# Kernel tuning notes

Measured on AMD Instinct MI355X. Metric: run time of the kernel, lower is better.

The kernel has to match this reference:

```python
import jax, jax.numpy as jnp
import numpy as np


def setup_inputs() -> dict:
    key = jax.random.key(0)
    k1, k2, k3, k4, k5 = jax.random.split(key, 5)
    B, K, S, E, I, D = 4, 2, 512, 8, 1024, 2048
    x = jax.random.normal(k1, (B, S, I), dtype=jnp.float32)
    weights = jax.random.uniform(k2, (B, K, S), dtype=jnp.float32)
    ensembles = jax.random.randint(k3, (B, K, S), 0, E, dtype=jnp.int64)
    # xavier_uniform-style init for expert weight tables
    lim1 = float(np.sqrt(6.0 / (D + I)))
    proj_in = jax.random.uniform(k4, (E, D, I), dtype=jnp.float32, minval=-lim1, maxval=lim1)
    proj_out = jax.random.uniform(k5, (E, I, D), dtype=jnp.float32, minval=-lim1, maxval=lim1)
    return {"x": x, "weights": weights, "ensembles": ensembles,
            "proj_in": proj_in, "proj_out": proj_out}


def reference(x, weights, ensembles, proj_in, proj_out):
    # x: (B,S,I); weights/ensembles: (B,K,S); proj_in: (E,D,I); proj_out: (E,I,D)
    # Same math as the torch module (dropout = identity in eval):
    #   per token t, out = sum_k w[k,t] * W2[e_kt] @ relu(W1[e_kt] @ x[t])
    # Computed as all-expert batched GEMMs + a gated (one-hot scatter) combine,
    # which is mathematically identical and avoids the (B,K,S,D,I) gather blowup.
    E = proj_in.shape[0]
    h = jax.nn.relu(jnp.einsum('edi,bsi->bsed', proj_in, x))      # (B,S,E,D)
    o = jnp.einsum('eid,bsed->bsei', proj_out, h)                 # (B,S,E,I)
    onehot = jax.nn.one_hot(ensembles, E, dtype=x.dtype)          # (B,K,S,E)
    gate = jnp.einsum('bks,bkse->bse', weights, onehot)           # (B,S,E)
    return jnp.einsum('bsei,bse->bsi', o, gate)                   # (B,S,I)
```

## Files before the change

### kernel.cpp

```cpp
#include <hip/hip_runtime.h>
#include <stdint.h>

#define THREADS 512
#define BM 256
#define BN 128
#define BK 64
#define MAXT 24
#define NE 8
#define BB 4
#define SS 512
#define KK 2
#define II 1024
#define DD 2048
#define NTOK (BB * SS)
#define NASSIGN (BB * KK * SS)

#define CH_X (NTOK * II / 8)
#define CH_P (NE * DD * II / 8)
#define CB_X (CH_X / 256)
#define CB_P (CH_P / 256)
#define CB_TOTAL (CB_X + 2 * CB_P)

typedef unsigned short u16;
typedef __attribute__((ext_vector_type(8))) __bf16 bf16x8;
typedef __attribute__((ext_vector_type(4))) float f32x4;
typedef __attribute__((ext_vector_type(4))) unsigned int u32x4;

__device__ __forceinline__ u16 f32_to_bf16(float f) {
    unsigned int u = __builtin_bit_cast(unsigned int, f);
    unsigned int r = u + 0x7FFFu + ((u >> 16) & 1u);
    return (u16)(r >> 16);
}

__device__ __forceinline__ void gload16(const void* g, void* l) {
    __builtin_amdgcn_global_load_lds(
        (const __attribute__((address_space(1))) unsigned int*)g,
        (__attribute__((address_space(3))) unsigned int*)l, 16, 0, 0);
}

__global__ void setup_kernel(const void* __restrict__ ens_raw,
                             const float* __restrict__ weights,
                             int* __restrict__ meta,
                             int* __restrict__ tok,
                             float* __restrict__ wgt) {
    __shared__ int s_cnt[NE];
    __shared__ int s_cur[NE];
    __shared__ int s_flag;
    const int t = threadIdx.x;
    if (t < NE) s_cnt[t] = 0;
    if (t == 0) s_flag = 0;
    __syncthreads();

    const unsigned int* w32 = (const unsigned int*)ens_raw;
    unsigned int f = 0;
    for (int i = t; i < NASSIGN / 2; i += 256) f |= w32[2 * i + 1];
    if (f) atomicOr(&s_flag, 1);
    __syncthreads();
    const bool is32 = (s_flag != 0);
    const int* e32 = (const int*)ens_raw;
    const long long* e64 = (const long long*)ens_raw;

    for (int a = t; a < NASSIGN; a += 256) {
        int e = is32 ? e32[a] : (int)e64[a];
        atomicAdd(&s_cnt[e & 7], 1);
    }
    __syncthreads();

    if (t == 0) {
        int pb = 0, nt = 0;
        for (int e = 0; e < NE; e++) {
            int c = s_cnt[e];
            meta[8 + e] = c;
            meta[16 + e] = pb;
            s_cur[e] = pb;
            int n128 = (c + 127) >> 7;
            int pe = pb + n128 * 128;
            for (int i2 = 0; i2 < n128; i2 += 2) {
                meta[32 + nt] = e;
                meta[64 + nt] = pb + i2 * 128;
                meta[96 + nt] = pb + c;
                meta[128 + nt] = pe;
                nt++;
            }
            pb = pe;
        }
        meta[0] = nt;
        meta[1] = pb;
    }
    __syncthreads();

    for (int a = t; a < NASSIGN; a += 256) {
        int e = is32 ? e32[a] : (int)e64[a];
        e &= 7;
        int slot = atomicAdd(&s_cur[e], 1);
        int b = a >> 10;
        int s = a & (SS - 1);
        tok[slot] = b * SS + s;
        wgt[slot] = weights[a];
    }
    __syncthreads();

    for (int e = 0; e < NE; e++) {
        int st = meta[16 + e] + meta[8 + e];
        int en = (e < NE - 1) ? meta[16 + e + 1] : meta[1];
        for (int i = st + t; i < en; i += 256) {
            tok[i] = 0;
            wgt[i] = 0.f;
        }
    }
}

__global__ __launch_bounds__(256)
void convert3(const float* __restrict__ x,
              const float* __restrict__ pin,
              const float* __restrict__ pout,
              u16* __restrict__ xb,
              u16* __restrict__ pb1,
              u16* __restrict__ pb2) {
    const int b = blockIdx.x;
    const float* s;
    u16* d;
    int base;
    if (b < CB_X)            { s = x;    d = xb;  base = b << 8; }
    else if (b < CB_X + CB_P){ s = pin;  d = pb1; base = (b - CB_X) << 8; }
    else                     { s = pout; d = pb2; base = (b - CB_X - CB_P) << 8; }
    const size_t k = (size_t)base + threadIdx.x;
    const f32x4* s4 = (const f32x4*)s;
    f32x4 a = __builtin_nontemporal_load(&s4[2 * k]);
    f32x4 c = __builtin_nontemporal_load(&s4[2 * k + 1]);
    union { u16 u[8]; u32x4 v; } o;
    o.u[0] = f32_to_bf16(a[0]); o.u[1] = f32_to_bf16(a[1]);
    o.u[2] = f32_to_bf16(a[2]); o.u[3] = f32_to_bf16(a[3]);
    o.u[4] = f32_to_bf16(c[0]); o.u[5] = f32_to_bf16(c[1]);
    o.u[6] = f32_to_bf16(c[2]); o.u[7] = f32_to_bf16(c[3]);
    *(u32x4*)(d + 8 * k) = o.v;
}

template <int MODE>
__global__ __launch_bounds__(THREADS, 2)
void gemm256(const u16* __restrict__ Abase,
             const u16* __restrict__ Bbase,
             const int* __restrict__ meta,
             const int* __restrict__ tok,
             const float* __restrict__ wgt,
             u16* __restrict__ hdst,
             float* __restrict__ outdst) {
    constexpr int Kdim = (MODE == 0) ? II : DD;
    constexpr int NT = Kdim / BK;
    __shared__ char smem[3 * 49152];

    const int lid = blockIdx.x;
    const int g = lid & 7;
    const int i = lid >> 3;
    const int tile = g * 3 + (i % 3);
    const int colt = i / 3;
    if (tile >= meta[0]) return;

    const int e     = meta[32 + tile];
    const int sbase = meta[64 + tile];
    const int rend  = meta[96 + tile];
    const int wend  = meta[128 + tile];
    const int padmax = meta[1];
    const int colbase = colt * BN;

    const int tid = threadIdx.x;
    const int lane = tid & 63;
    const int wv = tid >> 6;
    const int wr = wv >> 1;
    const int wc = wv & 1;

    const u16* Bp = Bbase + (size_t)e * (size_t)(DD * II) + (size_t)colbase * Kdim;

    int aoff[4], boff[2], adst[4], bdst[2];
#pragma unroll
    for (int j = 0; j < 4; j++) {
        int c = j * 512 + tid;
        int row = c >> 3;
        int s = (c & 7) ^ (row & 7);
        adst[j] = c * 16;
        int slot = sbase + row;
        if (slot > padmax - 1) slot = padmax - 1;
        aoff[j] = (MODE == 0 ? tok[slot] * II : slot * DD) + s * 8;
    }
#pragma unroll
    for (int j = 0; j < 2; j++) {
        int c = j * 512 + tid;
        int row = c >> 3;
        int s = (c & 7) ^ (row & 7);
        bdst[j] = c * 16;
        boff[j] = row * Kdim + s * 8;
    }

    f32x4 acc[4][4];
#pragma unroll
    for (int m = 0; m < 4; m++)
#pragma unroll
        for (int n = 0; n < 4; n++)
            acc[m][n] = (f32x4){0.f, 0.f, 0.f, 0.f};

    auto STAGE = [&](int kt, char* buf) {
        const int kof = kt * BK;
#pragma unroll
        for (int j = 0; j < 4; j++)
            gload16(Abase + aoff[j] + kof, buf + adst[j]);
#pragma unroll
        for (int j = 0; j < 2; j++)
            gload16(Bp + boff[j] + kof, buf + 32768 + bdst[j]);
    };

    auto COMPUTE = [&](const char* buf) {
        const u16* As = (const u16*)buf;
        const u16* Bs = (const u16*)(buf + 32768);
        bf16x8 a[2][4], b[2][4];
#pragma unroll
        for (int kk = 0; kk < 2; kk++) {
#pragma unroll
            for (int m = 0; m < 4; m++) {
                int row = wr * 64 + m * 16 + (lane & 15);
                int slot = (kk * 4 + (lane >> 4)) ^ (row & 7);
                a[kk][m] = *(const bf16x8*)&As[row * 64 + slot * 8];
            }
#pragma unroll
            for (int n = 0; n < 4; n++) {
                int col = wc * 64 + n * 16 + (lane & 15);
                int slot = (kk * 4 + (lane >> 4)) ^ (col & 7);
                b[kk][n] = *(const bf16x8*)&Bs[col * 64 + slot * 8];
            }
        }
        __builtin_amdgcn_s_setprio(1);
#pragma unroll
        for (int m = 0; m < 4; m++)
#pragma unroll
            for (int n = 0; n < 4; n++) {
                acc[m][n] = __builtin_amdgcn_mfma_f32_16x16x32_bf16(
                    a[0][m], b[0][n], acc[m][n], 0, 0, 0);
                acc[m][n] = __builtin_amdgcn_mfma_f32_16x16x32_bf16(
                    a[1][m], b[1][n], acc[m][n], 0, 0, 0);
            }
        __builtin_amdgcn_s_setprio(0);
    };

    char* pA = smem;
    char* pB = smem + 49152;
    char* pC = smem + 98304;

    STAGE(0, pA);
    STAGE(1, pB);
    asm volatile("s_waitcnt vmcnt(6)" ::: "memory");
    __builtin_amdgcn_sched_barrier(0);
    __builtin_amdgcn_s_barrier();
    __builtin_amdgcn_sched_barrier(0);

#pragma unroll 1
    for (int t = 0; t < NT; ++t) {
        if (t + 2 < NT) STAGE(t + 2, pC);
        COMPUTE(pA);
        if (t + 2 < NT) {
            asm volatile("s_waitcnt vmcnt(6)" ::: "memory");
        } else if (t + 1 < NT) {
            asm volatile("s_waitcnt vmcnt(0)" ::: "memory");
        }
        __builtin_amdgcn_sched_barrier(0);
        __builtin_amdgcn_s_barrier();
        __builtin_amdgcn_sched_barrier(0);
        char* tmp = pA; pA = pB; pB = pC; pC = tmp;
    }

    if (MODE == 0) {
#pragma unroll
        for (int m = 0; m < 4; m++) {
#pragma unroll
            for (int r = 0; r < 4; r++) {
                int row = wr * 64 + m * 16 + (lane >> 4) * 4 + r;
                int slot = sbase + row;
                if (slot < wend) {
                    size_t ro = (size_t)slot * DD;
#pragma unroll
                    for (int n = 0; n < 4; n++) {
                        int col = colbase + wc * 64 + n * 16 + (lane & 15);
                        float v = acc[m][n][r];
                        v = v > 0.f ? v : 0.f;
                        hdst[ro + col] = f32_to_bf16(v);
                    }
                }
            }
        }
    } else {
#pragma unroll
        for (int m = 0; m < 4; m++) {
#pragma unroll
            for (int r = 0; r < 4; r++) {
                int row = wr * 64 + m * 16 + (lane >> 4) * 4 + r;
                int slot = sbase + row;
                if (slot < rend) {
                    float w = wgt[slot];
                    size_t obase = (size_t)tok[slot] * II;
#pragma unroll
                    for (int n = 0; n < 4; n++) {
                        int col = colbase + wc * 64 + n * 16 + (lane & 15);
                        atomicAdd(&outdst[obase + col], acc[m][n][r] * w);
                    }
                }
            }
        }
    }
}

extern "C" void kernel_launch(void* const* d_in, const int* in_sizes, int n_in,
                              void* d_out, int out_size, void* d_ws, size_t ws_size,
                              hipStream_t stream) {
    const float* x = (const float*)d_in[0];
    const float* weights = (const float*)d_in[1];
    const void* ens = d_in[2];
    const float* pin = (const float*)d_in[3];
    const float* pout = (const float*)d_in[4];
    float* out = (float*)d_out;

    char* ws = (char*)d_ws;
    int*   meta    = (int*)(ws);
    int*   tok     = (int*)(ws + 1024);
    float* wgt     = (float*)(ws + 21504);
    u16*   x_bf    = (u16*)(ws + 41984);
    u16*   pin_bf  = (u16*)(ws + 4236288);
    u16*   pout_bf = (u16*)(ws + 37790720);
    u16*   h       = (u16*)(ws + 71345152);

    setup_kernel<<<dim3(1), dim3(256), 0, stream>>>(ens, weights, meta, tok, wgt);

    hipMemsetAsync(d_out, 0, (size_t)out_size * sizeof(float), stream);

    convert3<<<dim3(CB_TOTAL), dim3(256), 0, stream>>>(x, pin, pout, x_bf, pin_bf, pout_bf);

    gemm256<0><<<dim3(8 * 3 * 16), dim3(THREADS), 0, stream>>>(
        x_bf, pin_bf, meta, tok, wgt, h, nullptr);

    gemm256<1><<<dim3(8 * 3 * 8), dim3(THREADS), 0, stream>>>(
        h, pout_bf, meta, tok, wgt, nullptr, out);
}
```

Before: 134.8 us.

## Fuse setup into convert, loop tiles per expert, narrow second GEMM tiles

```diff
diff --git a/kernel.cpp b/kernel.cpp
--- a/kernel.cpp
+++ b/kernel.cpp
@@ -3,9 +3,7 @@
 
 #define THREADS 512
 #define BM 256
-#define BN 128
 #define BK 64
-#define MAXT 24
 #define NE 8
 #define BB 4
 #define SS 512
@@ -17,9 +15,9 @@
 
 #define CH_X (NTOK * II / 8)
 #define CH_P (NE * DD * II / 8)
-#define CB_X (CH_X / 256)
-#define CB_P (CH_P / 256)
-#define CB_TOTAL (CB_X + 2 * CB_P)
+#define CVB_X (CH_X / 512)
+#define CVB_P (CH_P / 512)
+#define CVB_TOTAL (CVB_X + 2 * CVB_P)
 
 typedef unsigned short u16;
 typedef __attribute__((ext_vector_type(8))) __bf16 bf16x8;
@@ -38,11 +36,16 @@
         (__attribute__((address_space(3))) unsigned int*)l, 16, 0, 0);
 }
 
-__global__ void setup_kernel(const void* __restrict__ ens_raw,
-                             const float* __restrict__ weights,
-                             int* __restrict__ meta,
-                             int* __restrict__ tok,
-                             float* __restrict__ wgt) {
+#define BARRIER() do { \
+    __builtin_amdgcn_sched_barrier(0); \
+    __builtin_amdgcn_s_barrier(); \
+    __builtin_amdgcn_sched_barrier(0); } while (0)
+
+__device__ void setup_body(const void* __restrict__ ens_raw,
+                           const float* __restrict__ weights,
+                           int* __restrict__ meta,
+                           int* __restrict__ tok,
+                           float* __restrict__ wgt) {
     __shared__ int s_cnt[NE];
     __shared__ int s_cur[NE];
     __shared__ int s_flag;
@@ -73,15 +76,18 @@
             meta[8 + e] = c;
             meta[16 + e] = pb;
             s_cur[e] = pb;
+            meta[160 + e] = nt;
             int n128 = (c + 127) >> 7;
             int pe = pb + n128 * 128;
+            int te = 0;
             for (int i2 = 0; i2 < n128; i2 += 2) {
                 meta[32 + nt] = e;
                 meta[64 + nt] = pb + i2 * 128;
                 meta[96 + nt] = pb + c;
                 meta[128 + nt] = pe;
-                nt++;
-            }
+                nt++; te++;
+            }
+            meta[168 + e] = te;
             pb = pe;
         }
         meta[0] = nt;
@@ -111,32 +117,48 @@
 }
 
 __global__ __launch_bounds__(256)
-void convert3(const float* __restrict__ x,
-              const float* __restrict__ pin,
-              const float* __restrict__ pout,
-              u16* __restrict__ xb,
-              u16* __restrict__ pb1,
-              u16* __restrict__ pb2) {
+void convert_setup(const float* __restrict__ x,
+                   const float* __restrict__ pin,
+                   const float* __restrict__ pout,
+                   u16* __restrict__ xb,
+                   u16* __restrict__ pb1,
+                   u16* __restrict__ pb2,
+                   const void* __restrict__ ens,
+                   const float* __restrict__ weights,
+                   int* __restrict__ meta,
+                   int* __restrict__ tok,
+                   float* __restrict__ wgt) {
     const int b = blockIdx.x;
+    if (b >= CVB_TOTAL) {
+        setup_body(ens, weights, meta, tok, wgt);
+        return;
+    }
     const float* s;
     u16* d;
-    int base;
-    if (b < CB_X)            { s = x;    d = xb;  base = b << 8; }
-    else if (b < CB_X + CB_P){ s = pin;  d = pb1; base = (b - CB_X) << 8; }
-    else                     { s = pout; d = pb2; base = (b - CB_X - CB_P) << 8; }
-    const size_t k = (size_t)base + threadIdx.x;
+    size_t rel;
+    if (b < CVB_X)             { s = x;    d = xb;  rel = (size_t)b * 512; }
+    else if (b < CVB_X + CVB_P){ s = pin;  d = pb1; rel = (size_t)(b - CVB_X) * 512; }
+    else                       { s = pout; d = pb2; rel = (size_t)(b - CVB_X - CVB_P) * 512; }
+    const size_t k = rel + (size_t)threadIdx.x * 2;
     const f32x4* s4 = (const f32x4*)s;
-    f32x4 a = __builtin_nontemporal_load(&s4[2 * k]);
-    f32x4 c = __builtin_nontemporal_load(&s4[2 * k + 1]);
-    union { u16 u[8]; u32x4 v; } o;
-    o.u[0] = f32_to_bf16(a[0]); o.u[1] = f32_to_bf16(a[1]);
-    o.u[2] = f32_to_bf16(a[2]); o.u[3] = f32_to_bf16(a[3]);
-    o.u[4] = f32_to_bf16(c[0]); o.u[5] = f32_to_bf16(c[1]);
-    o.u[6] = f32_to_bf16(c[2]); o.u[7] = f32_to_bf16(c[3]);
-    *(u32x4*)(d + 8 * k) = o.v;
-}
-
-template <int MODE>
+    f32x4 a0 = __builtin_nontemporal_load(&s4[2 * k]);
+    f32x4 a1 = __builtin_nontemporal_load(&s4[2 * k + 1]);
+    f32x4 a2 = __builtin_nontemporal_load(&s4[2 * k + 2]);
+    f32x4 a3 = __builtin_nontemporal_load(&s4[2 * k + 3]);
+    union { u16 u[8]; u32x4 v; } o0, o1;
+    o0.u[0] = f32_to_bf16(a0[0]); o0.u[1] = f32_to_bf16(a0[1]);
+    o0.u[2] = f32_to_bf16(a0[2]); o0.u[3] = f32_to_bf16(a0[3]);
+    o0.u[4] = f32_to_bf16(a1[0]); o0.u[5] = f32_to_bf16(a1[1]);
+    o0.u[6] = f32_to_bf16(a1[2]); o0.u[7] = f32_to_bf16(a1[3]);
+    o1.u[0] = f32_to_bf16(a2[0]); o1.u[1] = f32_to_bf16(a2[1]);
+    o1.u[2] = f32_to_bf16(a2[2]); o1.u[3] = f32_to_bf16(a2[3]);
+    o1.u[4] = f32_to_bf16(a3[0]); o1.u[5] = f32_to_bf16(a3[1]);
+    o1.u[6] = f32_to_bf16(a3[2]); o1.u[7] = f32_to_bf16(a3[3]);
+    *(u32x4*)(d + 8 * k) = o0.v;
+    *(u32x4*)(d + 8 * k + 8) = o1.v;
+}
+
+template <int MODE, int NB>
 __global__ __launch_bounds__(THREADS, 2)
 void gemm256(const u16* __restrict__ Abase,
              const u16* __restrict__ Bbase,
@@ -147,158 +169,168 @@
              float* __restrict__ outdst) {
     constexpr int Kdim = (MODE == 0) ? II : DD;
     constexpr int NT = Kdim / BK;
-    __shared__ char smem[3 * 49152];
+    constexpr int ASZ = BM * BK * 2;
+    constexpr int BSZ = NB * BK * 2;
+    constexpr int BUFSZ = ASZ + BSZ;
+    constexpr int IB = NB / 64;
+    constexpr int NF = NB / 32;
+    __shared__ char smem[3 * BUFSZ];
 
     const int lid = blockIdx.x;
     const int g = lid & 7;
     const int i = lid >> 3;
-    const int tile = g * 3 + (i % 3);
-    const int colt = i / 3;
-    if (tile >= meta[0]) return;
-
-    const int e     = meta[32 + tile];
-    const int sbase = meta[64 + tile];
-    const int rend  = meta[96 + tile];
-    const int wend  = meta[128 + tile];
-    const int padmax = meta[1];
-    const int colbase = colt * BN;
+    const int lt = i & 3;
+    const int colt = i >> 2;
+    const int tb   = meta[160 + g];
+    const int tcnt = meta[168 + g];
+    const int colbase = colt * NB;
 
     const int tid = threadIdx.x;
     const int lane = tid & 63;
     const int wv = tid >> 6;
     const int wr = wv >> 1;
     const int wc = wv & 1;
-
-    const u16* Bp = Bbase + (size_t)e * (size_t)(DD * II) + (size_t)colbase * Kdim;
-
-    int aoff[4], boff[2], adst[4], bdst[2];
-#pragma unroll
-    for (int j = 0; j < 4; j++) {
+    const int padmax = meta[1];
+
+    const u16* Bp = Bbase + (size_t)g * (size_t)(DD * II) + (size_t)colbase * Kdim;
+
+    int boff[IB], bdst[IB];
+#pragma unroll
+    for (int j = 0; j < IB; j++) {
         int c = j * 512 + tid;
-        int row = c >> 3;
-        int s = (c & 7) ^ (row & 7);
-        adst[j] = c * 16;
-        int slot = sbase + row;
-        if (slot > padmax - 1) slot = padmax - 1;
-        aoff[j] = (MODE == 0 ? tok[slot] * II : slot * DD) + s * 8;
-    }
-#pragma unroll
-    for (int j = 0; j < 2; j++) {
-        int c = j * 512 + tid;
-        int row = c >> 3;
-        int s = (c & 7) ^ (row & 7);
+        int col = c >> 3;
+        int s = (c & 7) ^ (col & 7);
         bdst[j] = c * 16;
-        boff[j] = row * Kdim + s * 8;
-    }
-
-    f32x4 acc[4][4];
-#pragma unroll
-    for (int m = 0; m < 4; m++)
-#pragma unroll
-        for (int n = 0; n < 4; n++)
-            acc[m][n] = (f32x4){0.f, 0.f, 0.f, 0.f};
-
-    auto STAGE = [&](int kt, char* buf) {
-        const int kof = kt * BK;
-#pragma unroll
-        for (int j = 0; j < 4; j++)
-            gload16(Abase + aoff[j] + kof, buf + adst[j]);
-#pragma unroll
-        for (int j = 0; j < 2; j++)
-            gload16(Bp + boff[j] + kof, buf + 32768 + bdst[j]);
-    };
-
-    auto COMPUTE = [&](const char* buf) {
-        const u16* As = (const u16*)buf;
-        const u16* Bs = (const u16*)(buf + 32768);
-        bf16x8 a[2][4], b[2][4];
-#pragma unroll
-        for (int kk = 0; kk < 2; kk++) {
+        boff[j] = col * Kdim + s * 8;
+    }
+
+    for (int tile = tb + lt; tile < tb + tcnt; tile += 4) {
+        const int sbase = meta[64 + tile];
+        const int rend  = meta[96 + tile];
+        const int wend  = meta[128 + tile];
+
+        int aoff[4], adst[4];
+#pragma unroll
+        for (int j = 0; j < 4; j++) {
+            int c = j * 512 + tid;
+            int row = c >> 3;
+            int s = (c & 7) ^ (row & 7);
+            adst[j] = c * 16;
+            int slot = sbase + row;
+            if (slot > padmax - 1) slot = padmax - 1;
+            aoff[j] = (MODE == 0 ? tok[slot] * II : slot * DD) + s * 8;
+        }
+
+        f32x4 acc[4][NF];
+#pragma unroll
+        for (int m = 0; m < 4; m++)
+#pragma unroll
+            for (int n = 0; n < NF; n++)
+                acc[m][n] = (f32x4){0.f, 0.f, 0.f, 0.f};
+
+        auto STAGE = [&](int kt, char* buf) {
+            const int kof = kt * BK;
+#pragma unroll
+            for (int j = 0; j < 4; j++)
+                gload16(Abase + aoff[j] + kof, buf + adst[j]);
+#pragma unroll
+            for (int j = 0; j < IB; j++)
+                gload16(Bp + boff[j] + kof, buf + ASZ + bdst[j]);
+        };
+
+        auto COMPUTE = [&](const char* buf) {
+            const u16* As = (const u16*)buf;
+            const u16* Bs = (const u16*)(buf + ASZ);
+            bf16x8 a[2][4], b[2][NF];
+#pragma unroll
+            for (int kk = 0; kk < 2; kk++) {
+#pragma unroll
+                for (int m = 0; m < 4; m++) {
+                    int row = wr * 64 + m * 16 + (lane & 15);
+                    int slot = (kk * 4 + (lane >> 4)) ^ (row & 7);
+                    a[kk][m] = *(const bf16x8*)&As[row * 64 + slot * 8];
+                }
+#pragma unroll
+                for (int n = 0; n < NF; n++) {
+                    int col = wc * (NB / 2) + n * 16 + (lane & 15);
+                    int slot = (kk * 4 + (lane >> 4)) ^ (col & 7);
+                    b[kk][n] = *(const bf16x8*)&Bs[col * 64 + slot * 8];
+                }
+            }
+            asm volatile("s_waitcnt lgkmcnt(0)" ::: "memory");
+            __builtin_amdgcn_sched_barrier(0);
+            __builtin_amdgcn_s_setprio(1);
+#pragma unroll
+            for (int m = 0; m < 4; m++)
+#pragma unroll
+                for (int n = 0; n < NF; n++) {
+                    acc[m][n] = __builtin_amdgcn_mfma_f32_16x16x32_bf16(
+                        a[0][m], b[0][n], acc[m][n], 0, 0, 0);
+                    acc[m][n] = __builtin_amdgcn_mfma_f32_16x16x32_bf16(
+                        a[1][m], b[1][n], acc[m][n], 0, 0, 0);
+                }
+            __builtin_amdgcn_s_setprio(0);
+        };
+
+        char* pA = smem;
+        char* pB = smem + BUFSZ;
+        char* pC = smem + 2 * BUFSZ;
+
+        STAGE(0, pA);
+        STAGE(1, pB);
+        if constexpr (IB == 2) asm volatile("s_waitcnt vmcnt(6)" ::: "memory");
+        else                   asm volatile("s_waitcnt vmcnt(5)" ::: "memory");
+        BARRIER();
+
+#pragma unroll 1
+        for (int t = 0; t < NT; ++t) {
+            const bool st = (t + 2 < NT);
+            if (st) STAGE(t + 2, pC);
+            COMPUTE(pA);
+            if (st) {
+                if constexpr (IB == 2) asm volatile("s_waitcnt vmcnt(6)" ::: "memory");
+                else                   asm volatile("s_waitcnt vmcnt(5)" ::: "memory");
+            } else if (t + 1 < NT) {
+                asm volatile("s_waitcnt vmcnt(0)" ::: "memory");
+            }
+            BARRIER();
+            { char* tp = pA; pA = pB; pB = pC; pC = tp; }
+        }
+
+        if (MODE == 0) {
 #pragma unroll
             for (int m = 0; m < 4; m++) {
-                int row = wr * 64 + m * 16 + (lane & 15);
-                int slot = (kk * 4 + (lane >> 4)) ^ (row & 7);
-                a[kk][m] = *(const bf16x8*)&As[row * 64 + slot * 8];
-            }
-#pragma unroll
-            for (int n = 0; n < 4; n++) {
-                int col = wc * 64 + n * 16 + (lane & 15);
-                int slot = (kk * 4 + (lane >> 4)) ^ (col & 7);
-                b[kk][n] = *(const bf16x8*)&Bs[col * 64 + slot * 8];
-            }
-        }
-        __builtin_amdgcn_s_setprio(1);
-#pragma unroll
-        for (int m = 0; m < 4; m++)
-#pragma unroll
-            for (int n = 0; n < 4; n++) {
-                acc[m][n] = __builtin_amdgcn_mfma_f32_16x16x32_bf16(
-                    a[0][m], b[0][n], acc[m][n], 0, 0, 0);
-                acc[m][n] = __builtin_amdgcn_mfma_f32_16x16x32_bf16(
-                    a[1][m], b[1][n], acc[m][n], 0, 0, 0);
-            }
-        __builtin_amdgcn_s_setprio(0);
-    };
-
-    char* pA = smem;
-    char* pB = smem + 49152;
-    char* pC = smem + 98304;
-
-    STAGE(0, pA);
-    STAGE(1, pB);
-    asm volatile("s_waitcnt vmcnt(6)" ::: "memory");
-    __builtin_amdgcn_sched_barrier(0);
-    __builtin_amdgcn_s_barrier();
-    __builtin_amdgcn_sched_barrier(0);
-
-#pragma unroll 1
-    for (int t = 0; t < NT; ++t) {
-        if (t + 2 < NT) STAGE(t + 2, pC);
-        COMPUTE(pA);
-        if (t + 2 < NT) {
-            asm volatile("s_waitcnt vmcnt(6)" ::: "memory");
-        } else if (t + 1 < NT) {
-            asm volatile("s_waitcnt vmcnt(0)" ::: "memory");
-        }
-        __builtin_amdgcn_sched_barrier(0);
-        __builtin_amdgcn_s_barrier();
-        __builtin_amdgcn_sched_barrier(0);
-        char* tmp = pA; pA = pB; pB = pC; pC = tmp;
-    }
-
-    if (MODE == 0) {
-#pragma unroll
-        for (int m = 0; m < 4; m++) {
-#pragma unroll
-            for (int r = 0; r < 4; r++) {
-                int row = wr * 64 + m * 16 + (lane >> 4) * 4 + r;
-                int slot = sbase + row;
-                if (slot < wend) {
-                    size_t ro = (size_t)slot * DD;
-#pragma unroll
-                    for (int n = 0; n < 4; n++) {
-                        int col = colbase + wc * 64 + n * 16 + (lane & 15);
-                        float v = acc[m][n][r];
-                        v = v > 0.f ? v : 0.f;
-                        hdst[ro + col] = f32_to_bf16(v);
+#pragma unroll
+                for (int r = 0; r < 4; r++) {
+                    int row = wr * 64 + m * 16 + (lane >> 4) * 4 + r;
+                    int slot = sbase + row;
+                    if (slot < wend) {
+                        size_t ro = (size_t)slot * DD;
+#pragma unroll
+                        for (int n = 0; n < NF; n++) {
+                            int col = colbase + wc * (NB / 2) + n * 16 + (lane & 15);
+                            float v = acc[m][n][r];
+                            v = v > 0.f ? v : 0.f;
+                            hdst[ro + col] = f32_to_bf16(v);
+                        }
                     }
                 }
             }
-        }
-    } else {
-#pragma unroll
-        for (int m = 0; m < 4; m++) {
-#pragma unroll
-            for (int r = 0; r < 4; r++) {
-                int row = wr * 64 + m * 16 + (lane >> 4) * 4 + r;
-                int slot = sbase + row;
-                if (slot < rend) {
-                    float w = wgt[slot];
-                    size_t obase = (size_t)tok[slot] * II;
-#pragma unroll
-                    for (int n = 0; n < 4; n++) {
-                        int col = colbase + wc * 64 + n * 16 + (lane & 15);
-                        atomicAdd(&outdst[obase + col], acc[m][n][r] * w);
+        } else {
+#pragma unroll
+            for (int m = 0; m < 4; m++) {
+#pragma unroll
+                for (int r = 0; r < 4; r++) {
+                    int row = wr * 64 + m * 16 + (lane >> 4) * 4 + r;
+                    int slot = sbase + row;
+                    if (slot < rend) {
+                        float w = wgt[slot];
+                        size_t obase = (size_t)tok[slot] * II;
+#pragma unroll
+                        for (int n = 0; n < NF; n++) {
+                            int col = colbase + wc * (NB / 2) + n * 16 + (lane & 15);
+                            atomicAdd(&outdst[obase + col], acc[m][n][r] * w);
+                        }
                     }
                 }
             }
@@ -325,15 +357,14 @@
     u16*   pout_bf = (u16*)(ws + 37790720);
     u16*   h       = (u16*)(ws + 71345152);
 
-    setup_kernel<<<dim3(1), dim3(256), 0, stream>>>(ens, weights, meta, tok, wgt);
-
     hipMemsetAsync(d_out, 0, (size_t)out_size * sizeof(float), stream);
 
-    convert3<<<dim3(CB_TOTAL), dim3(256), 0, stream>>>(x, pin, pout, x_bf, pin_bf, pout_bf);
-
-    gemm256<0><<<dim3(8 * 3 * 16), dim3(THREADS), 0, stream>>>(
+    convert_setup<<<dim3(CVB_TOTAL + 1), dim3(256), 0, stream>>>(
+        x, pin, pout, x_bf, pin_bf, pout_bf, ens, weights, meta, tok, wgt);
+
+    gemm256<0, 128><<<dim3(512), dim3(THREADS), 0, stream>>>(
         x_bf, pin_bf, meta, tok, wgt, h, nullptr);
 
-    gemm256<1><<<dim3(8 * 3 * 8), dim3(THREADS), 0, stream>>>(
+    gemm256<1, 64><<<dim3(512), dim3(THREADS), 0, stream>>>(
         h, pout_bf, meta, tok, wgt, nullptr, out);
 }
```

Result: slower. 163.7 us (+21.5%).

## Enlarge first GEMM tile to 256x256, fuse setup into conversion kernel

Applied to the files above, without the earlier changes.

```diff
diff --git a/kernel.cpp b/kernel.cpp
--- a/kernel.cpp
+++ b/kernel.cpp
@@ -2,10 +2,6 @@
 #include <stdint.h>
 
 #define THREADS 512
-#define BM 256
-#define BN 128
-#define BK 64
-#define MAXT 24
 #define NE 8
 #define BB 4
 #define SS 512
@@ -15,11 +11,11 @@
 #define NTOK (BB * SS)
 #define NASSIGN (BB * KK * SS)
 
-#define CH_X (NTOK * II / 8)
-#define CH_P (NE * DD * II / 8)
-#define CB_X (CH_X / 256)
-#define CB_P (CH_P / 256)
-#define CB_TOTAL (CB_X + 2 * CB_P)
+#define F4_X (NTOK * II / 4)
+#define F4_P (NE * DD * II / 4)
+#define CVB_X (F4_X / 1024)
+#define CVB_P (F4_P / 1024)
+#define CVB_TOTAL (CVB_X + 2 * CVB_P)
 
 typedef unsigned short u16;
 typedef __attribute__((ext_vector_type(8))) __bf16 bf16x8;
@@ -32,17 +28,26 @@
     return (u16)(r >> 16);
 }
 
+__device__ __forceinline__ unsigned int pk2(float a, float b) {
+    return (unsigned int)f32_to_bf16(a) | ((unsigned int)f32_to_bf16(b) << 16);
+}
+
 __device__ __forceinline__ void gload16(const void* g, void* l) {
     __builtin_amdgcn_global_load_lds(
         (const __attribute__((address_space(1))) unsigned int*)g,
         (__attribute__((address_space(3))) unsigned int*)l, 16, 0, 0);
 }
 
-__global__ void setup_kernel(const void* __restrict__ ens_raw,
-                             const float* __restrict__ weights,
-                             int* __restrict__ meta,
-                             int* __restrict__ tok,
-                             float* __restrict__ wgt) {
+#define BARRIER() do { \
+    __builtin_amdgcn_sched_barrier(0); \
+    __builtin_amdgcn_s_barrier(); \
+    __builtin_amdgcn_sched_barrier(0); } while (0)
+
+__device__ void setup_body(const void* __restrict__ ens_raw,
+                           const float* __restrict__ weights,
+                           int* __restrict__ meta,
+                           int* __restrict__ tok,
+                           float* __restrict__ wgt) {
     __shared__ int s_cnt[NE];
     __shared__ int s_cur[NE];
     __shared__ int s_flag;
@@ -111,57 +116,198 @@
 }
 
 __global__ __launch_bounds__(256)
-void convert3(const float* __restrict__ x,
-              const float* __restrict__ pin,
-              const float* __restrict__ pout,
-              u16* __restrict__ xb,
-              u16* __restrict__ pb1,
-              u16* __restrict__ pb2) {
+void convert_setup(const float* __restrict__ x,
+                   const float* __restrict__ pin,
+                   const float* __restrict__ pout,
+                   u16* __restrict__ xb,
+                   u16* __restrict__ pb1,
+                   u16* __restrict__ pb2,
+                   const void* __restrict__ ens,
+                   const float* __restrict__ weights,
+                   int* __restrict__ meta,
+                   int* __restrict__ tok,
+                   float* __restrict__ wgt) {
     const int b = blockIdx.x;
+    if (b >= CVB_TOTAL) {
+        setup_body(ens, weights, meta, tok, wgt);
+        return;
+    }
     const float* s;
     u16* d;
-    int base;
-    if (b < CB_X)            { s = x;    d = xb;  base = b << 8; }
-    else if (b < CB_X + CB_P){ s = pin;  d = pb1; base = (b - CB_X) << 8; }
-    else                     { s = pout; d = pb2; base = (b - CB_X - CB_P) << 8; }
-    const size_t k = (size_t)base + threadIdx.x;
+    size_t base;
+    if (b < CVB_X)             { s = x;    d = xb;  base = (size_t)b * 1024; }
+    else if (b < CVB_X + CVB_P){ s = pin;  d = pb1; base = (size_t)(b - CVB_X) * 1024; }
+    else                       { s = pout; d = pb2; base = (size_t)(b - CVB_X - CVB_P) * 1024; }
     const f32x4* s4 = (const f32x4*)s;
-    f32x4 a = __builtin_nontemporal_load(&s4[2 * k]);
-    f32x4 c = __builtin_nontemporal_load(&s4[2 * k + 1]);
-    union { u16 u[8]; u32x4 v; } o;
-    o.u[0] = f32_to_bf16(a[0]); o.u[1] = f32_to_bf16(a[1]);
-    o.u[2] = f32_to_bf16(a[2]); o.u[3] = f32_to_bf16(a[3]);
-    o.u[4] = f32_to_bf16(c[0]); o.u[5] = f32_to_bf16(c[1]);
-    o.u[6] = f32_to_bf16(c[2]); o.u[7] = f32_to_bf16(c[3]);
-    *(u32x4*)(d + 8 * k) = o.v;
-}
-
-template <int MODE>
+    f32x4 v[4];
+#pragma unroll
+    for (int q = 0; q < 4; q++)
+        v[q] = __builtin_nontemporal_load(&s4[base + q * 256 + threadIdx.x]);
+#pragma unroll
+    for (int q = 0; q < 4; q++) {
+        uint2 o;
+        o.x = pk2(v[q][0], v[q][1]);
+        o.y = pk2(v[q][2], v[q][3]);
+        *(uint2*)(d + 4 * (base + q * 256 + threadIdx.x)) = o;
+    }
+}
+
 __global__ __launch_bounds__(THREADS, 2)
-void gemm256(const u16* __restrict__ Abase,
-             const u16* __restrict__ Bbase,
-             const int* __restrict__ meta,
-             const int* __restrict__ tok,
-             const float* __restrict__ wgt,
-             u16* __restrict__ hdst,
-             float* __restrict__ outdst) {
-    constexpr int Kdim = (MODE == 0) ? II : DD;
-    constexpr int NT = Kdim / BK;
-    __shared__ char smem[3 * 49152];
+void gemm1(const u16* __restrict__ Abase,
+           const u16* __restrict__ Bbase,
+           const int* __restrict__ meta,
+           const int* __restrict__ tok,
+           u16* __restrict__ hdst) {
+    constexpr int NT = II / 64;
+    constexpr int ASZ = 256 * 64 * 2;
+    constexpr int BUFSZ = 2 * ASZ;
+    __shared__ char smem[2 * BUFSZ];
 
     const int lid = blockIdx.x;
     const int g = lid & 7;
     const int i = lid >> 3;
-    const int tile = g * 3 + (i % 3);
+    const int tile = g + 8 * (i % 3);
+    const int colt = i / 3;
+    if (tile >= meta[0]) return;
+
+    const int e     = meta[32 + tile];
+    const int sbase = meta[64 + tile];
+    const int wend  = meta[128 + tile];
+    const int padmax = meta[1];
+    const int colbase = colt * 256;
+
+    const int tid = threadIdx.x;
+    const int lane = tid & 63;
+    const int wv = tid >> 6;
+    const int wr = wv >> 2;
+    const int wc = wv & 3;
+
+    const u16* Bp = Bbase + (size_t)e * (size_t)(DD * II) + (size_t)colbase * II;
+
+    int aoff[4], boff[4], cdst[4];
+#pragma unroll
+    for (int j = 0; j < 4; j++) {
+        int c = j * 512 + tid;
+        int row = c >> 3;
+        int s = (c & 7) ^ (row & 7);
+        cdst[j] = c * 16;
+        int slot = sbase + row;
+        if (slot > padmax - 1) slot = padmax - 1;
+        aoff[j] = tok[slot] * II + s * 8;
+        boff[j] = row * II + s * 8;
+    }
+
+    f32x4 acc[8][4];
+#pragma unroll
+    for (int m = 0; m < 8; m++)
+#pragma unroll
+        for (int n = 0; n < 4; n++)
+            acc[m][n] = (f32x4){0.f, 0.f, 0.f, 0.f};
+
+    auto STAGE = [&](int kt, char* buf) {
+        const int kof = kt * 64;
+#pragma unroll
+        for (int j = 0; j < 4; j++)
+            gload16(Abase + aoff[j] + kof, buf + cdst[j]);
+#pragma unroll
+        for (int j = 0; j < 4; j++)
+            gload16(Bp + boff[j] + kof, buf + ASZ + cdst[j]);
+    };
+
+    auto COMPUTE = [&](const char* buf) {
+        const u16* As = (const u16*)buf;
+        const u16* Bs = (const u16*)(buf + ASZ);
+#pragma unroll
+        for (int kk = 0; kk < 2; kk++) {
+            bf16x8 a[8], b[4];
+#pragma unroll
+            for (int m = 0; m < 8; m++) {
+                int row = wr * 128 + m * 16 + (lane & 15);
+                int slot = (kk * 4 + (lane >> 4)) ^ (row & 7);
+                a[m] = *(const bf16x8*)&As[row * 64 + slot * 8];
+            }
+#pragma unroll
+            for (int n = 0; n < 4; n++) {
+                int col = wc * 64 + n * 16 + (lane & 15);
+                int slot = (kk * 4 + (lane >> 4)) ^ (col & 7);
+                b[n] = *(const bf16x8*)&Bs[col * 64 + slot * 8];
+            }
+            asm volatile("s_waitcnt lgkmcnt(0)" ::: "memory");
+            __builtin_amdgcn_sched_barrier(0);
+            __builtin_amdgcn_s_setprio(1);
+#pragma unroll
+            for (int m = 0; m < 8; m++)
+#pragma unroll
+                for (int n = 0; n < 4; n++)
+                    acc[m][n] = __builtin_amdgcn_mfma_f32_16x16x32_bf16(
+                        a[m], b[n], acc[m][n], 0, 0, 0);
+            __builtin_amdgcn_s_setprio(0);
+        }
+    };
+
+    char* buf0 = smem;
+    char* buf1 = smem + BUFSZ;
+
+    STAGE(0, buf0);
+    asm volatile("s_waitcnt vmcnt(0)" ::: "memory");
+    BARRIER();
+
+#pragma unroll 1
+    for (int t = 0; t < NT; ++t) {
+        char* cur = (t & 1) ? buf1 : buf0;
+        char* nxt = (t & 1) ? buf0 : buf1;
+        const bool st = (t + 1 < NT);
+        if (st) STAGE(t + 1, nxt);
+        COMPUTE(cur);
+        if (st) asm volatile("s_waitcnt vmcnt(0)" ::: "memory");
+        BARRIER();
+    }
+
+#pragma unroll
+    for (int m = 0; m < 8; m++) {
+#pragma unroll
+        for (int r = 0; r < 4; r++) {
+            int row = wr * 128 + m * 16 + (lane >> 4) * 4 + r;
+            int slot = sbase + row;
+            if (slot < wend) {
+                size_t ro = (size_t)slot * DD;
+#pragma unroll
+                for (int n = 0; n < 4; n++) {
+                    int col = colbase + wc * 64 + n * 16 + (lane & 15);
+                    float v = acc[m][n][r];
+                    v = v > 0.f ? v : 0.f;
+                    hdst[ro + col] = f32_to_bf16(v);
+                }
+            }
+        }
+    }
+}
+
+__global__ __launch_bounds__(THREADS, 2)
+void gemm2(const u16* __restrict__ Abase,
+           const u16* __restrict__ Bbase,
+           const int* __restrict__ meta,
+           const int* __restrict__ tok,
+           const float* __restrict__ wgt,
+           float* __restrict__ outdst) {
+    constexpr int NT = DD / 64;
+    constexpr int ASZ = 256 * 64 * 2;
+    constexpr int BSZ = 128 * 64 * 2;
+    constexpr int BUFSZ = ASZ + BSZ;
+    __shared__ char smem[3 * BUFSZ];
+
+    const int lid = blockIdx.x;
+    const int g = lid & 7;
+    const int i = lid >> 3;
+    const int tile = g + 8 * (i % 3);
     const int colt = i / 3;
     if (tile >= meta[0]) return;
 
     const int e     = meta[32 + tile];
     const int sbase = meta[64 + tile];
     const int rend  = meta[96 + tile];
-    const int wend  = meta[128 + tile];
     const int padmax = meta[1];
-    const int colbase = colt * BN;
+    const int colbase = colt * 128;
 
     const int tid = threadIdx.x;
     const int lane = tid & 63;
@@ -169,9 +315,9 @@
     const int wr = wv >> 1;
     const int wc = wv & 1;
 
-    const u16* Bp = Bbase + (size_t)e * (size_t)(DD * II) + (size_t)colbase * Kdim;
-
-    int aoff[4], boff[2], adst[4], bdst[2];
+    const u16* Bp = Bbase + (size_t)e * (size_t)(DD * II) + (size_t)colbase * DD;
+
+    int aoff[4], adst[4], boff[2], bdst[2];
 #pragma unroll
     for (int j = 0; j < 4; j++) {
         int c = j * 512 + tid;
@@ -180,7 +326,7 @@
         adst[j] = c * 16;
         int slot = sbase + row;
         if (slot > padmax - 1) slot = padmax - 1;
-        aoff[j] = (MODE == 0 ? tok[slot] * II : slot * DD) + s * 8;
+        aoff[j] = slot * DD + s * 8;
     }
 #pragma unroll
     for (int j = 0; j < 2; j++) {
@@ -188,7 +334,7 @@
         int row = c >> 3;
         int s = (c & 7) ^ (row & 7);
         bdst[j] = c * 16;
-        boff[j] = row * Kdim + s * 8;
+        boff[j] = row * DD + s * 8;
     }
 
     f32x4 acc[4][4];
@@ -199,18 +345,18 @@
             acc[m][n] = (f32x4){0.f, 0.f, 0.f, 0.f};
 
     auto STAGE = [&](int kt, char* buf) {
-        const int kof = kt * BK;
+        const int kof = kt * 64;
 #pragma unroll
         for (int j = 0; j < 4; j++)
             gload16(Abase + aoff[j] + kof, buf + adst[j]);
 #pragma unroll
         for (int j = 0; j < 2; j++)
-            gload16(Bp + boff[j] + kof, buf + 32768 + bdst[j]);
+            gload16(Bp + boff[j] + kof, buf + ASZ + bdst[j]);
     };
 
     auto COMPUTE = [&](const char* buf) {
         const u16* As = (const u16*)buf;
-        const u16* Bs = (const u16*)(buf + 32768);
+        const u16* Bs = (const u16*)(buf + ASZ);
         bf16x8 a[2][4], b[2][4];
 #pragma unroll
         for (int kk = 0; kk < 2; kk++) {
@@ -227,6 +373,8 @@
                 b[kk][n] = *(const bf16x8*)&Bs[col * 64 + slot * 8];
             }
         }
+        asm volatile("s_waitcnt lgkmcnt(0)" ::: "memory");
+        __builtin_amdgcn_sched_barrier(0);
         __builtin_amdgcn_s_setprio(1);
 #pragma unroll
         for (int m = 0; m < 4; m++)
@@ -241,65 +389,41 @@
     };
 
     char* pA = smem;
-    char* pB = smem + 49152;
-    char* pC = smem + 98304;
+    char* pB = smem + BUFSZ;
+    char* pC = smem + 2 * BUFSZ;
 
     STAGE(0, pA);
     STAGE(1, pB);
     asm volatile("s_waitcnt vmcnt(6)" ::: "memory");
-    __builtin_amdgcn_sched_barrier(0);
-    __builtin_amdgcn_s_barrier();
-    __builtin_amdgcn_sched_barrier(0);
+    BARRIER();
 
 #pragma unroll 1
     for (int t = 0; t < NT; ++t) {
-        if (t + 2 < NT) STAGE(t + 2, pC);
+        const bool st = (t + 2 < NT);
+        if (st) STAGE(t + 2, pC);
         COMPUTE(pA);
-        if (t + 2 < NT) {
+        if (st) {
             asm volatile("s_waitcnt vmcnt(6)" ::: "memory");
         } else if (t + 1 < NT) {
             asm volatile("s_waitcnt vmcnt(0)" ::: "memory");
         }
-        __builtin_amdgcn_sched_barrier(0);
-        __builtin_amdgcn_s_barrier();
-        __builtin_amdgcn_sched_barrier(0);
-        char* tmp = pA; pA = pB; pB = pC; pC = tmp;
-    }
-
-    if (MODE == 0) {
-#pragma unroll
-        for (int m = 0; m < 4; m++) {
-#pragma unroll
-            for (int r = 0; r < 4; r++) {
-                int row = wr * 64 + m * 16 + (lane >> 4) * 4 + r;
-                int slot = sbase + row;
-                if (slot < wend) {
-                    size_t ro = (size_t)slot * DD;
-#pragma unroll
-                    for (int n = 0; n < 4; n++) {
-                        int col = colbase + wc * 64 + n * 16 + (lane & 15);
-                        float v = acc[m][n][r];
-                        v = v > 0.f ? v : 0.f;
-                        hdst[ro + col] = f32_to_bf16(v);
-                    }
-                }
-            }
-        }
-    } else {
-#pragma unroll
-        for (int m = 0; m < 4; m++) {
-#pragma unroll
-            for (int r = 0; r < 4; r++) {
-                int row = wr * 64 + m * 16 + (lane >> 4) * 4 + r;
-                int slot = sbase + row;
-                if (slot < rend) {
-                    float w = wgt[slot];
-                    size_t obase = (size_t)tok[slot] * II;
-#pragma unroll
-                    for (int n = 0; n < 4; n++) {
-                        int col = colbase + wc * 64 + n * 16 + (lane & 15);
-                        atomicAdd(&outdst[obase + col], acc[m][n][r] * w);
-                    }
+        BARRIER();
+        { char* tp = pA; pA = pB; pB = pC; pC = tp; }
+    }
+
+#pragma unroll
+    for (int m = 0; m < 4; m++) {
+#pragma unroll
+        for (int r = 0; r < 4; r++) {
+            int row = wr * 64 + m * 16 + (lane >> 4) * 4 + r;
+            int slot = sbase + row;
+            if (slot < rend) {
+                float w = wgt[slot];
+                size_t obase = (size_t)tok[slot] * II;
+#pragma unroll
+                for (int n = 0; n < 4; n++) {
+                    int col = colbase + wc * 64 + n * 16 + (lane & 15);
+                    atomicAdd(&outdst[obase + col], acc[m][n][r] * w);
                 }
             }
         }
@@ -325,15 +449,14 @@
     u16*   pout_bf = (u16*)(ws + 37790720);
     u16*   h       = (u16*)(ws + 71345152);
 
-    setup_kernel<<<dim3(1), dim3(256), 0, stream>>>(ens, weights, meta, tok, wgt);
-
     hipMemsetAsync(d_out, 0, (size_t)out_size * sizeof(float), stream);
 
-    convert3<<<dim3(CB_TOTAL), dim3(256), 0, stream>>>(x, pin, pout, x_bf, pin_bf, pout_bf);
-
-    gemm256<0><<<dim3(8 * 3 * 16), dim3(THREADS), 0, stream>>>(
-        x_bf, pin_bf, meta, tok, wgt, h, nullptr);
-
-    gemm256<1><<<dim3(8 * 3 * 8), dim3(THREADS), 0, stream>>>(
-        h, pout_bf, meta, tok, wgt, nullptr, out);
-}
+    convert_setup<<<dim3(CVB_TOTAL + 1), dim3(256), 0, stream>>>(
+        x, pin, pout, x_bf, pin_bf, pout_bf, ens, weights, meta, tok, wgt);
+
+    gemm1<<<dim3(8 * 3 * 8), dim3(THREADS), 0, stream>>>(
+        x_bf, pin_bf, meta, tok, h);
+
+    gemm2<<<dim3(8 * 3 * 8), dim3(THREADS), 0, stream>>>(
+        h, pout_bf, meta, tok, wgt, out);
+}
```

New measurement: 126.1 us. 1.07x faster.
